# Performance work log

Measured on AMD Instinct MI355X. Metric: run time of the kernel, lower is better.

The kernel has to match this reference:

```python
import jax, jax.numpy as jnp
import numpy as np

N = 100000   # nodes
E = 1600000  # edges
D = 128      # input_dim == hidden_dim
L = 4        # n_layers
G = 128      # num graphs
NC = 10      # n_classes
EPS = 1e-5


def setup_inputs() -> dict:
    key = jax.random.key(0)
    ks = jax.random.split(key, 12)
    x = jax.random.normal(ks[0], (N, D), jnp.float32)
    edge_index = jax.random.randint(ks[1], (2, E), 0, N, dtype=jnp.int64)
    batch = jnp.sort(jax.random.randint(ks[2], (N,), 0, G, dtype=jnp.int64))
    s = 1.0 / np.sqrt(D)
    conv_w = jax.random.normal(ks[3], (L, D, D), jnp.float32) * s
    conv_b = jnp.zeros((L, D), jnp.float32)
    gn_weight = jnp.ones((L, D), jnp.float32)
    gn_bias = jnp.zeros((L, D), jnp.float32)
    gn_mean_scale = jnp.ones((L, D), jnp.float32)
    dense_w1 = jax.random.normal(ks[4], (D, D), jnp.float32) * s
    dense_b1 = jnp.zeros((D,), jnp.float32)
    bn_gamma = jnp.ones((D,), jnp.float32)
    bn_beta = jnp.zeros((D,), jnp.float32)
    bn_mean = jnp.zeros((D,), jnp.float32)   # running stats (eval mode)
    bn_var = jnp.ones((D,), jnp.float32)
    dense_w2 = jax.random.normal(ks[5], (D, NC), jnp.float32) * s
    dense_b2 = jnp.zeros((NC,), jnp.float32)
    return dict(x=x, edge_index=edge_index, batch=batch, conv_w=conv_w,
                conv_b=conv_b, gn_weight=gn_weight, gn_bias=gn_bias,
                gn_mean_scale=gn_mean_scale, dense_w1=dense_w1, dense_b1=dense_b1,
                bn_gamma=bn_gamma, bn_beta=bn_beta, bn_mean=bn_mean, bn_var=bn_var,
                dense_w2=dense_w2, dense_b2=dense_b2)


def _graph_norm(x, batch, counts, weight, bias, mean_scale):
    # PyG GraphNorm: (x - alpha*mean) / sqrt(var + eps) * weight + bias, per graph
    mean = jax.ops.segment_sum(x, batch, num_segments=G) / counts        # [G, D]
    sub = x - mean_scale * mean[batch]                                    # [N, D]
    var = jax.ops.segment_sum(sub * sub, batch, num_segments=G) / counts  # [G, D]
    return weight * sub * jax.lax.rsqrt(var + EPS)[batch] + bias


def reference(x, edge_index, batch, conv_w, conv_b, gn_weight, gn_bias,
              gn_mean_scale, dense_w1, dense_b1, bn_gamma, bn_beta,
              bn_mean, bn_var, dense_w2, dense_b2):
    # GCNConv normalization with self-loops (symmetric D^-1/2 (A+I) D^-1/2)
    loop = jnp.arange(N, dtype=edge_index.dtype)
    src = jnp.concatenate([edge_index[0], loop])
    dst = jnp.concatenate([edge_index[1], loop])
    deg = jax.ops.segment_sum(jnp.ones((E + N,), x.dtype), dst, num_segments=N)
    dis = jax.lax.rsqrt(deg)  # deg >= 1 due to self-loops
    nrm = (dis[src] * dis[dst])[:, None]                                  # [E+N, 1]
    counts = jax.ops.segment_sum(jnp.ones((N, 1), x.dtype), batch, num_segments=G)

    x_res = x  # input_dim == hidden_dim -> no input projection
    for i in range(L):
        h = x @ conv_w[i]                                # [N, D]
        h = jax.ops.segment_sum(h[src] * nrm, dst, num_segments=N) + conv_b[i]
        h = _graph_norm(h, batch, counts, gn_weight[i], gn_bias[i], gn_mean_scale[i])
        h = jax.nn.elu(h)
        # dropout: identity in eval mode
        x = h + x_res
        x_res = x

    pooled = jax.ops.segment_sum(x, batch, num_segments=G)  # global_add_pool [G, D]
    z = pooled @ dense_w1 + dense_b1
    z = bn_gamma * (z - bn_mean) * jax.lax.rsqrt(bn_var + EPS) + bn_beta
    z = jax.nn.relu(z)
    z = z @ dense_w2 + dense_b2
    return (x, z)
```

## Files before the change

kernel.cpp:

```cpp
#include <hip/hip_runtime.h>
#include <stdint.h>

#define N_NODES 100000
#define N_PAD   100032
#define N_EDGES 1600000
#define DIM 128
#define NLAYERS 4
#define NGRAPH 128
#define NCLS 10
#define EPSV 1e-5f
#define NSLOT 32

#define BIN_SHIFT 9
#define NBUCKET ((N_NODES + 511) >> 9)
#define P1_EPB 4096
#define P1_BLOCKS ((N_EDGES + P1_EPB - 1) / P1_EPB)

typedef __attribute__((ext_vector_type(8))) short short8_t;
typedef __attribute__((ext_vector_type(4))) float float4_t;


__device__ __forceinline__ float bf_lo(uint32_t u) { return __uint_as_float(u << 16); }
__device__ __forceinline__ float bf_hi(uint32_t u) { return __uint_as_float(u & 0xffff0000u); }
__device__ __forceinline__ uint32_t f2bf_rne(float f) {
    uint32_t x = __float_as_uint(f);
    return (x + 0x7fffu + ((x >> 16) & 1u)) >> 16;
}
__device__ __forceinline__ uint32_t pack_bf2(float a, float b) {
    return f2bf_rne(a) | (f2bf_rne(b) << 16);
}
__device__ __forceinline__ float4 unpack4(uint2 u) {
    return make_float4(bf_lo(u.x), bf_hi(u.x), bf_lo(u.y), bf_hi(u.y));
}
__device__ __forceinline__ float ub0(uint32_t u) { return (float)( u        & 0xffu); }
__device__ __forceinline__ float ub1(uint32_t u) { return (float)((u >>  8) & 0xffu); }
__device__ __forceinline__ float ub2(uint32_t u) { return (float)((u >> 16) & 0xffu); }
__device__ __forceinline__ float ub3(uint32_t u) { return (float)( u >> 24        ); }
__device__ __forceinline__ float elu_neg(float x) { return __expf(x) - 1.f; }


__global__ void k_node_meta(const int* __restrict__ batch, int* __restrict__ gstart,
                            int* __restrict__ bcnt) {
    int i = blockIdx.x * blockDim.x + threadIdx.x;
    if (i < NBUCKET) bcnt[i] = 0;
    if (i >= N_NODES) return;
    int b = batch[i];
    if (i == 0) {
        for (int g = 0; g <= b; g++) gstart[g] = 0;
    } else {
        int bp = batch[i - 1];
        for (int g = bp + 1; g <= b; g++) gstart[g] = i;
    }
    if (i == N_NODES - 1) {
        for (int g = b + 1; g <= NGRAPH; g++) gstart[g] = N_NODES;
    }
}

__global__ __launch_bounds__(256) void k_bhist(const int* __restrict__ ei, int* __restrict__ bcnt) {
    __shared__ int hist[NBUCKET];
    int t = threadIdx.x;
    for (int i = t; i < NBUCKET; i += 256) hist[i] = 0;
    __syncthreads();
    int e0 = blockIdx.x * P1_EPB;
    int e1 = e0 + P1_EPB; if (e1 > N_EDGES) e1 = N_EDGES;
    for (int e = e0 + t; e < e1; e += 256) atomicAdd(&hist[ei[N_EDGES + e] >> BIN_SHIFT], 1);
    __syncthreads();
    for (int i = t; i < NBUCKET; i += 256) if (hist[i]) atomicAdd(&bcnt[i], hist[i]);
}

__global__ __launch_bounds__(256) void k_bscan(const int* __restrict__ bcnt,
                                               int* __restrict__ bucket_off, int* __restrict__ bcur) {
    __shared__ int s[256];
    int t = threadIdx.x;
    int v = (t < NBUCKET) ? bcnt[t] : 0;
    s[t] = v; __syncthreads();
    for (int off = 1; off < 256; off <<= 1) {
        int a = (t >= off) ? s[t - off] : 0;
        __syncthreads();
        s[t] += a;
        __syncthreads();
    }
    if (t < NBUCKET) { bucket_off[t] = s[t] - v; bcur[t] = s[t] - v; }
    if (t == 0) bucket_off[NBUCKET] = s[255];
}

__global__ __launch_bounds__(256) void k_bin_edges(const int* __restrict__ ei,
                                                   int* __restrict__ bcur,
                                                   int2* __restrict__ binned) {
    __shared__ int hist[NBUCKET];
    __shared__ int base[NBUCKET];
    int t = threadIdx.x;
    int e0 = blockIdx.x * P1_EPB;
    int e1 = e0 + P1_EPB; if (e1 > N_EDGES) e1 = N_EDGES;
    for (int i = t; i < NBUCKET; i += 256) hist[i] = 0;
    __syncthreads();
    int myrank[P1_EPB / 256];
    int cnt = 0;
    for (int e = e0 + t; e < e1; e += 256) {
        int d = ei[N_EDGES + e];
        myrank[cnt++] = atomicAdd(&hist[d >> BIN_SHIFT], 1);
    }
    __syncthreads();
    for (int i = t; i < NBUCKET; i += 256) base[i] = atomicAdd(&bcur[i], hist[i]);
    __syncthreads();
    cnt = 0;
    for (int e = e0 + t; e < e1; e += 256) {
        int s = ei[e];
        int d = ei[N_EDGES + e];
        binned[base[d >> BIN_SHIFT] + myrank[cnt++]] = make_int2(s, d);
    }
}

__global__ __launch_bounds__(256) void k_bucket_build(const int2* __restrict__ binned,
                                                      const int* __restrict__ bucket_off,
                                                      int* __restrict__ rowoff,
                                                      float* __restrict__ dis,
                                                      int* __restrict__ psrc) {
    __shared__ int cnt[512];
    __shared__ int sa[512];
    __shared__ int sb[512];
    int b = blockIdx.x;
    int t = threadIdx.x;
    int n0 = b << BIN_SHIFT;
    int j0 = bucket_off[b], j1 = bucket_off[b + 1];
    cnt[t] = 0; cnt[t + 256] = 0;
    __syncthreads();
    for (int j = j0 + t; j < j1; j += 256) atomicAdd(&cnt[binned[j].y & 511], 1);
    __syncthreads();
    sa[t] = cnt[t]; sa[t + 256] = cnt[t + 256];
    __syncthreads();
    int* A = sa; int* B = sb;
    for (int off = 1; off < 512; off <<= 1) {
        int i0 = t, i1 = t + 256;
        B[i0] = A[i0] + ((i0 >= off) ? A[i0 - off] : 0);
        B[i1] = A[i1] + ((i1 >= off) ? A[i1 - off] : 0);
        __syncthreads();
        int* tmp = A; A = B; B = tmp;
    }
    for (int i = t; i < 512; i += 256) {
        int n = n0 + i;
        if (n < N_NODES) {
            rowoff[n] = j0 + A[i] - cnt[i];
            dis[n] = rsqrtf((float)(1 + cnt[i]));
        }
    }
    if (b == NBUCKET - 1 && t == 0) rowoff[N_NODES] = N_EDGES;
    for (int idx = t; idx < 512 * NSLOT; idx += 256) {
        int i = idx >> 5, k = idx & (NSLOT - 1);
        int n = n0 + i;
        if (n < N_NODES && k >= cnt[i]) psrc[(size_t)n * NSLOT + k] = N_NODES;
    }
}

__global__ __launch_bounds__(256) void k_scatter(const int2* __restrict__ binned,
                                                 const float* __restrict__ dis,
                                                 const int* __restrict__ rowoff,
                                                 const int* __restrict__ bucket_off,
                                                 int2* __restrict__ csc,
                                                 int* __restrict__ psrc) {
    __shared__ int lcur[512];
    int b = blockIdx.x;
    int t = threadIdx.x;
    lcur[t] = 0; lcur[t + 256] = 0;
    __syncthreads();
    int j0 = bucket_off[b], j1 = bucket_off[b + 1];
    for (int j = j0 + t; j < j1; j += 256) {
        int2 sd = binned[j];
        float w = dis[sd.x] * dis[sd.y];
        int rank = atomicAdd(&lcur[sd.y & 511], 1);
        csc[rowoff[sd.y] + rank] = make_int2(sd.x, __float_as_int(w));
        if (rank < NSLOT) psrc[(size_t)sd.y * NSLOT + rank] = sd.x;
    }
}

__global__ void k_cast_w(const float* __restrict__ W, uint32_t* __restrict__ Wt) {
    int i = blockIdx.x * blockDim.x + threadIdx.x;
    if (i >= NLAYERS * DIM * 64) return;
    int l = i / (DIM * 64);
    int n = (i / 64) % DIM;
    int ku = i % 64;
    const float* Wl = W + (size_t)l * DIM * DIM;
    float w0 = Wl[(2 * ku) * DIM + n];
    float w1 = Wl[(2 * ku + 1) * DIM + n];
    Wt[i] = pack_bf2(w0, w1);
}


__device__ __forceinline__ void gemm_phase(const uint32_t (*atile)[68], const uint32_t* __restrict__ Wt,
                                           uint8_t (*ctile8)[132], float* rmaxl,
                                           uint8_t* __restrict__ H8,
                                           float* __restrict__ hsd, const float* __restrict__ dis,
                                           int blk, int t) {
    int wid = t >> 6;
    int lane = t & 63;
    int quad = lane >> 4;
    int s15 = lane & 15;

    float4_t acc[8];
#pragma unroll
    for (int i = 0; i < 8; i++) acc[i] = (float4_t){0.f, 0.f, 0.f, 0.f};

#pragma unroll
    for (int kk = 0; kk < 4; kk++) {
        uint4 au = *(const uint4*)&atile[wid * 16 + s15][quad * 4 + kk * 16];
        short8_t a = __builtin_bit_cast(short8_t, au);
#pragma unroll
        for (int nt = 0; nt < 8; nt++) {
            uint4 bu = *(const uint4*)(Wt + (size_t)(nt * 16 + s15) * 64 + kk * 16 + quad * 4);
            short8_t b = __builtin_bit_cast(short8_t, bu);
            acc[nt] = __builtin_amdgcn_mfma_f32_16x16x32_bf16(a, b, acc[nt], 0, 0, 0);
        }
    }
    __syncthreads();

    float sinv[4];
#pragma unroll
    for (int r = 0; r < 4; r++) {
        float m = fabsf(acc[0][r]);
#pragma unroll
        for (int nt = 1; nt < 8; nt++) m = fmaxf(m, fabsf(acc[nt][r]));
        m = fmaxf(m, __shfl_xor(m, 1));
        m = fmaxf(m, __shfl_xor(m, 2));
        m = fmaxf(m, __shfl_xor(m, 4));
        m = fmaxf(m, __shfl_xor(m, 8));
        if (s15 == 0) rmaxl[wid * 16 + quad * 4 + r] = m;
        sinv[r] = (m > 0.f) ? 127.f / m : 0.f;
    }
#pragma unroll
    for (int nt = 0; nt < 8; nt++) {
#pragma unroll
        for (int r = 0; r < 4; r++) {
            int qv = (int)fmaf(acc[nt][r], sinv[r], 128.5f);
            ctile8[wid * 16 + quad * 4 + r][nt * 16 + s15] = (uint8_t)qv;
        }
    }
    __syncthreads();
    uint8_t* Hb = H8 + (size_t)blk * 64 * 128;
    float* Hsb = hsd + (size_t)blk * 64;
#pragma unroll
    for (int i = 0; i < 8; i++) {
        int idx = t + 256 * i;
        int row = idx >> 5, cu = idx & 31;
        uint32_t v = *(const uint32_t*)&ctile8[row][cu * 4];
        ((uint32_t*)Hb)[(size_t)row * 32 + cu] = v;
        if (cu == 0) {
            size_t gr = (size_t)blk * 64 + row;
            float dv = (gr < N_NODES) ? dis[gr] : 0.f;
            Hsb[row] = rmaxl[row] * (1.f / 127.f) * dv;
        }
    }
}

#define GEMM_SMEM \
    __shared__ __align__(16) char smem[64 * 68 * 4]; \
    uint32_t (*atile)[68] = (uint32_t(*)[68])smem; \
    uint8_t (*ctile8)[132] = (uint8_t(*)[132])smem; \
    float* rmaxl = (float*)(smem + 64 * 132);

__global__ __launch_bounds__(256) void k_gemm0(const float* __restrict__ X, const uint32_t* __restrict__ Wt,
                                               uint8_t* __restrict__ H8, float* __restrict__ hsd,
                                               const float* __restrict__ dis) {
    GEMM_SMEM
    int t = threadIdx.x;
    size_t row0 = (size_t)blockIdx.x * 64;
#pragma unroll
    for (int i = 0; i < 8; i++) {
        int idx = t + 256 * i;
        int row = idx >> 5, q = idx & 31;
        size_t gr = row0 + row;
        uint2 p = make_uint2(0u, 0u);
        if (gr < N_NODES) {
            float4 v = ((const float4*)(X + gr * DIM))[q];
            p.x = pack_bf2(v.x, v.y);
            p.y = pack_bf2(v.z, v.w);
        }
        *(uint2*)&atile[row][q * 2] = p;
    }
    __syncthreads();
    gemm_phase(atile, Wt, ctile8, rmaxl, H8, hsd, dis, blockIdx.x, t);
}

template <bool RBF>
__global__ __launch_bounds__(256) void k_norm_gemm(const uint32_t* __restrict__ A, const int* __restrict__ batch,
                                                   const float* __restrict__ amean, const float* __restrict__ rstd,
                                                   const float* __restrict__ gw, const float* __restrict__ gb,
                                                   const void* __restrict__ res, uint32_t* __restrict__ res_out,
                                                   const uint32_t* __restrict__ Wt,
                                                   uint8_t* __restrict__ H8, float* __restrict__ hsd,
                                                   const float* __restrict__ dis) {
    GEMM_SMEM
    int t = threadIdx.x;
    size_t row0 = (size_t)blockIdx.x * 64;
#pragma unroll
    for (int i = 0; i < 8; i++) {
        int idx = t + 256 * i;
        int row = idx >> 5, q = idx & 31;
        size_t gr = row0 + row;
        uint2 p = make_uint2(0u, 0u);
        if (gr < N_NODES) {
            int g = batch[gr];
            float4 v = unpack4(((const uint2*)(A + gr * 64))[q]);
            float4 am = ((const float4*)amean)[g * 32 + q];
            float4 rs = ((const float4*)rstd)[g * 32 + q];
            float4 w = ((const float4*)gw)[q];
            float4 b = ((const float4*)gb)[q];
            float4 r;
            if (RBF) r = unpack4(((const uint2*)((const uint32_t*)res + gr * 64))[q]);
            else     r = ((const float4*)res)[gr * 32 + q];
            float4 o;
            o.x = w.x * (v.x - am.x) * rs.x + b.x;
            o.y = w.y * (v.y - am.y) * rs.y + b.y;
            o.z = w.z * (v.z - am.z) * rs.z + b.z;
            o.w = w.w * (v.w - am.w) * rs.w + b.w;
            o.x = ((o.x > 0.f) ? o.x : elu_neg(o.x)) + r.x;
            o.y = ((o.y > 0.f) ? o.y : elu_neg(o.y)) + r.y;
            o.z = ((o.z > 0.f) ? o.z : elu_neg(o.z)) + r.z;
            o.w = ((o.w > 0.f) ? o.w : elu_neg(o.w)) + r.w;
            p.x = pack_bf2(o.x, o.y);
            p.y = pack_bf2(o.z, o.w);
            ((uint2*)(res_out + gr * 64))[q] = p;
        }
        *(uint2*)&atile[row][q * 2] = p;
    }
    __syncthreads();
    gemm_phase(atile, Wt, ctile8, rmaxl, H8, hsd, dis, blockIdx.x, t);
}


#define ACC8(WS, U) \
    acc[0] += WS * ub0(U.x); acc[1] += WS * ub1(U.x); \
    acc[2] += WS * ub2(U.x); acc[3] += WS * ub3(U.x); \
    acc[4] += WS * ub0(U.y); acc[5] += WS * ub1(U.y); \
    acc[6] += WS * ub2(U.y); acc[7] += WS * ub3(U.y);

__global__ __launch_bounds__(256, 4) void k_aggregate(const uint8_t* __restrict__ H8,
                                                      const float* __restrict__ hsd,
                                                      const int* __restrict__ psrc,
                                                      const int2* __restrict__ csc,
                                                      const int* __restrict__ rowoff,
                                                      const float* __restrict__ dis,
                                                      const float* __restrict__ bias,
                                                      uint32_t* __restrict__ Out) {
    int wid = threadIdx.x >> 6;
    int lane = threadIdx.x & 63;
    uint32_t q = (uint32_t)(lane >> 4);
    uint32_t s = (uint32_t)(lane & 15);
    uint32_t n = (uint32_t)blockIdx.x * 4u + (uint32_t)wid;
    uint32_t s8 = s << 3;

    float dd = dis[n];
    const int4* P = (const int4*)(psrc + ((size_t)n << 5) + (q << 3));
    int4 pa = P[0];
    int4 pb = P[1];
    float hn = hsd[n];
    uint2 us = *(const uint2*)(H8 + ((n << 7) | s8));
    int b0 = rowoff[n], b1 = rowoff[n + 1];

    float h0 = hsd[(uint32_t)pa.x];
    float h1 = hsd[(uint32_t)pa.y];
    float h2 = hsd[(uint32_t)pa.z];
    float h3 = hsd[(uint32_t)pa.w];
    float h4 = hsd[(uint32_t)pb.x];
    float h5 = hsd[(uint32_t)pb.y];
    float h6 = hsd[(uint32_t)pb.z];
    float h7 = hsd[(uint32_t)pb.w];
    uint2 u0 = *(const uint2*)(H8 + (((uint32_t)pa.x << 7) | s8));
    uint2 u1 = *(const uint2*)(H8 + (((uint32_t)pa.y << 7) | s8));
    uint2 u2 = *(const uint2*)(H8 + (((uint32_t)pa.z << 7) | s8));
    uint2 u3 = *(const uint2*)(H8 + (((uint32_t)pa.w << 7) | s8));
    uint2 u4 = *(const uint2*)(H8 + (((uint32_t)pb.x << 7) | s8));
    uint2 u5 = *(const uint2*)(H8 + (((uint32_t)pb.y << 7) | s8));
    uint2 u6 = *(const uint2*)(H8 + (((uint32_t)pb.z << 7) | s8));
    uint2 u7 = *(const uint2*)(H8 + (((uint32_t)pb.w << 7) | s8));

    float ws0 = dd * h0, ws1 = dd * h1, ws2 = dd * h2, ws3 = dd * h3;
    float ws4 = dd * h4, ws5 = dd * h5, ws6 = dd * h6, ws7 = dd * h7;

    float sw = (q == 0) ? dd * hn : 0.f;
    float acc[8];
    acc[0] = sw * ub0(us.x); acc[1] = sw * ub1(us.x);
    acc[2] = sw * ub2(us.x); acc[3] = sw * ub3(us.x);
    acc[4] = sw * ub0(us.y); acc[5] = sw * ub1(us.y);
    acc[6] = sw * ub2(us.y); acc[7] = sw * ub3(us.y);
    float offs = sw;

    ACC8(ws0, u0); ACC8(ws1, u1); ACC8(ws2, u2); ACC8(ws3, u3);
    ACC8(ws4, u4); ACC8(ws5, u5); ACC8(ws6, u6); ACC8(ws7, u7);
    offs += ws0 + ws1 + ws2 + ws3 + ws4 + ws5 + ws6 + ws7;

    if (b1 - b0 > NSLOT) {
        for (int j = b0 + NSLOT + (int)q; j < b1; j += 4) {
            uint32_t sx = (uint32_t)csc[j].x;
            float w = dd * hsd[sx];
            uint2 u = *(const uint2*)(H8 + ((sx << 7) | s8));
            ACC8(w, u);
            offs += w;
        }
    }

#pragma unroll
    for (int k = 0; k < 8; k++) {
        acc[k] += __shfl_xor(acc[k], 16);
        acc[k] += __shfl_xor(acc[k], 32);
    }
    offs += __shfl_xor(offs, 16);
    offs += __shfl_xor(offs, 32);
    float o0 = (q == 0) ? acc[0] : (q == 1) ? acc[2] : (q == 2) ? acc[4] : acc[6];
    float o1 = (q == 0) ? acc[1] : (q == 1) ? acc[3] : (q == 2) ? acc[5] : acc[7];
    float corr = -128.f * offs;
    float2 bb = ((const float2*)bias)[s * 4 + q];
    Out[(n << 6) | (s * 4 + q)] = pack_bf2(o0 + corr + bb.x, o1 + corr + bb.y);
}

__global__ __launch_bounds__(512) void k_stats(const uint32_t* __restrict__ A, const int* __restrict__ gstart,
                                               const float* __restrict__ mscale,
                                               float* __restrict__ amean, float* __restrict__ rstd) {
    __shared__ float L1[8][DIM];
    __shared__ float L2[8][DIM];
    int g = blockIdx.x;
    int t = threadIdx.x;
    int f2 = t & 63;
    int p = t >> 6;
    int s0 = gstart[g], s1 = gstart[g + 1];
    float sa = 0.f, sb = 0.f, qa = 0.f, qb = 0.f;
    for (int n = s0 + p; n < s1; n += 8) {
        uint32_t u = A[(size_t)n * 64 + f2];
        float a = bf_lo(u), b = bf_hi(u);
        sa += a; qa += a * a;
        sb += b; qb += b * b;
    }
    L1[p][2 * f2] = sa; L1[p][2 * f2 + 1] = sb;
    L2[p][2 * f2] = qa; L2[p][2 * f2 + 1] = qb;
    __syncthreads();
    if (t < DIM) {
        float s = 0.f, s2 = 0.f;
#pragma unroll
        for (int i = 0; i < 8; i++) { s += L1[i][t]; s2 += L2[i][t]; }
        int cnt = s1 - s0;
        float inv = (cnt > 0) ? 1.0f / (float)cnt : 0.f;
        float m = s * inv;
        float a = mscale[t];
        float var = s2 * inv - (2.f * a - a * a) * m * m;
        amean[g * DIM + t] = a * m;
        rstd[g * DIM + t] = rsqrtf(var + EPSV);
    }
}

__global__ __launch_bounds__(512) void k_pool_head(const uint32_t* __restrict__ A,
                                                   const uint32_t* __restrict__ resb,
                                                   const int* __restrict__ gstart,
                                                   const float* __restrict__ amean, const float* __restrict__ rstd,
                                                   const float* __restrict__ gw, const float* __restrict__ gb,
                                                   const float* __restrict__ w1, const float* __restrict__ b1,
                                                   const float* __restrict__ gamma, const float* __restrict__ beta,
                                                   const float* __restrict__ rmean, const float* __restrict__ rvar,
                                                   const float* __restrict__ w2, const float* __restrict__ b2,
                                                   float* __restrict__ outx, float* __restrict__ zout) {
    __shared__ float L[8][DIM];
    __shared__ float sp[DIM];
    __shared__ float sz[DIM];
    int g = blockIdx.x, t = threadIdx.x;
    int f2 = t & 63;
    int p = t >> 6;
    int s0 = gstart[g], s1 = gstart[g + 1];
    float am0 = amean[g * DIM + 2 * f2], am1 = amean[g * DIM + 2 * f2 + 1];
    float rs0 = rstd[g * DIM + 2 * f2],  rs1 = rstd[g * DIM + 2 * f2 + 1];
    float w0_ = gw[2 * f2], w1_ = gw[2 * f2 + 1];
    float b0_ = gb[2 * f2], b1_ = gb[2 * f2 + 1];
    float p0 = 0.f, p1 = 0.f;
    for (int n = s0 + p; n < s1; n += 8) {
        uint32_t u = A[(size_t)n * 64 + f2];
        uint32_t ur = resb[(size_t)n * 64 + f2];
        float a = bf_lo(u), b = bf_hi(u);
        float r0 = bf_lo(ur), r1 = bf_hi(ur);
        float o0 = w0_ * (a - am0) * rs0 + b0_;
        float o1 = w1_ * (b - am1) * rs1 + b1_;
        o0 = ((o0 > 0.f) ? o0 : elu_neg(o0)) + r0;
        o1 = ((o1 > 0.f) ? o1 : elu_neg(o1)) + r1;
        ((float2*)(outx + (size_t)n * DIM))[f2] = make_float2(o0, o1);
        p0 += o0; p1 += o1;
    }
    L[p][2 * f2] = p0; L[p][2 * f2 + 1] = p1;
    __syncthreads();
    if (t < DIM) {
        float s = 0.f;
#pragma unroll
        for (int i = 0; i < 8; i++) s += L[i][t];
        sp[t] = s;
    }
    __syncthreads();
    if (t < DIM) {
        float acc = b1[t];
#pragma unroll 8
        for (int k = 0; k < DIM; k++) acc += sp[k] * w1[k * DIM + t];
        acc = gamma[t] * (acc - rmean[t]) * rsqrtf(rvar[t] + EPSV) + beta[t];
        sz[t] = fmaxf(acc, 0.f);
    }
    __syncthreads();
    if (t < NCLS) {
        float a2 = b2[t];
#pragma unroll 8
        for (int k = 0; k < DIM; k++) a2 += sz[k] * w2[k * NCLS + t];
        zout[g * NCLS + t] = a2;
    }
}


extern "C" void kernel_launch(void* const* d_in, const int* in_sizes, int n_in,
                              void* d_out, int out_size, void* d_ws, size_t ws_size,
                              hipStream_t stream) {
    const float* x_in   = (const float*)d_in[0];
    const int*   ei     = (const int*)d_in[1];
    const int*   batch  = (const int*)d_in[2];
    const float* conv_w = (const float*)d_in[3];
    const float* conv_b = (const float*)d_in[4];
    const float* gn_w   = (const float*)d_in[5];
    const float* gn_b   = (const float*)d_in[6];
    const float* gn_ms  = (const float*)d_in[7];
    const float* w1     = (const float*)d_in[8];
    const float* b1     = (const float*)d_in[9];
    const float* bng    = (const float*)d_in[10];
    const float* bnb    = (const float*)d_in[11];
    const float* bnm    = (const float*)d_in[12];
    const float* bnv    = (const float*)d_in[13];
    const float* w2     = (const float*)d_in[14];
    const float* b2     = (const float*)d_in[15];

    float* out_x = (float*)d_out;
    float* out_z = out_x + (size_t)N_NODES * DIM;

    char* ws = (char*)d_ws;
    size_t off = 0;
    auto alloc = [&](size_t bytes) -> void* {
        void* p = ws + off;
        off += (bytes + 255) / 256 * 256;
        return p;
    };
    uint8_t* h8      = (uint8_t*)alloc(sizeof(uint8_t) * (size_t)N_PAD * 128);
    float*   hsd     = (float*)alloc(sizeof(float) * (size_t)N_PAD);
    uint32_t* agg    = (uint32_t*)alloc(sizeof(uint32_t) * (size_t)N_NODES * 64);
    uint32_t* resb   = (uint32_t*)alloc(sizeof(uint32_t) * (size_t)N_NODES * 64);
    int2*  csc       = (int2*)alloc(sizeof(int2) * (size_t)N_EDGES);
    int2*  binned    = (int2*)alloc(sizeof(int2) * (size_t)N_EDGES);
    int*   psrc      = (int*)alloc(sizeof(int) * (size_t)N_NODES * NSLOT);
    uint32_t* wt     = (uint32_t*)alloc(sizeof(uint32_t) * NLAYERS * DIM * 64);
    float* dis       = (float*)alloc(sizeof(float) * N_NODES);
    int*   rowoff    = (int*)alloc(sizeof(int) * (N_NODES + 1));
    int*   bcnt      = (int*)alloc(sizeof(int) * NBUCKET);
    int*   boffb     = (int*)alloc(sizeof(int) * (NBUCKET + 1));
    int*   bcur      = (int*)alloc(sizeof(int) * NBUCKET);
    int*   gstart    = (int*)alloc(sizeof(int) * (NGRAPH + 1));
    float* amean     = (float*)alloc(sizeof(float) * NGRAPH * DIM);
    float* rstd      = (float*)alloc(sizeof(float) * NGRAPH * DIM);

    k_node_meta<<<(N_NODES + 255) / 256, 256, 0, stream>>>(batch, gstart, bcnt);
    k_bhist<<<P1_BLOCKS, 256, 0, stream>>>(ei, bcnt);
    k_bscan<<<1, 256, 0, stream>>>(bcnt, boffb, bcur);
    k_bin_edges<<<P1_BLOCKS, 256, 0, stream>>>(ei, bcur, binned);
    k_bucket_build<<<NBUCKET, 256, 0, stream>>>(binned, boffb, rowoff, dis, psrc);
    k_scatter<<<NBUCKET, 256, 0, stream>>>(binned, dis, rowoff, boffb, csc, psrc);
    k_cast_w<<<(NLAYERS * DIM * 64 + 255) / 256, 256, 0, stream>>>(conv_w, wt);

    k_gemm0<<<N_PAD / 64, 256, 0, stream>>>(x_in, wt, h8, hsd, dis);
    for (int l = 0; l < NLAYERS; l++) {
        k_aggregate<<<N_NODES / 4, 256, 0, stream>>>(h8, hsd, psrc, csc, rowoff, dis,
                                                     conv_b + (size_t)l * DIM, agg);
        k_stats<<<NGRAPH, 512, 0, stream>>>(agg, gstart, gn_ms + (size_t)l * DIM, amean, rstd);
        if (l == 0) {
            k_norm_gemm<false><<<N_PAD / 64, 256, 0, stream>>>(agg, batch, amean, rstd, gn_w, gn_b,
                                                               (const void*)x_in, resb,
                                                               wt + (size_t)1 * DIM * 64, h8, hsd, dis);
        } else if (l < NLAYERS - 1) {
            k_norm_gemm<true><<<N_PAD / 64, 256, 0, stream>>>(agg, batch, amean, rstd,
                                                              gn_w + (size_t)l * DIM, gn_b + (size_t)l * DIM,
                                                              (const void*)resb, resb,
                                                              wt + (size_t)(l + 1) * DIM * 64, h8, hsd, dis);
        } else {
            k_pool_head<<<NGRAPH, 512, 0, stream>>>(agg, resb, gstart, amean, rstd,
                                                    gn_w + (size_t)l * DIM, gn_b + (size_t)l * DIM,
                                                    w1, b1, bng, bnb, bnm, bnv, w2, b2, out_x, out_z);
        }
    }
}
```

Baseline: 771.9 us.

## Process two nodes per wavefront in aggregation and fold self-loop into padded slots

```diff
diff --git a/kernel.cpp b/kernel.cpp
--- a/kernel.cpp
+++ b/kernel.cpp
@@ -148,7 +148,7 @@
     for (int idx = t; idx < 512 * NSLOT; idx += 256) {
         int i = idx >> 5, k = idx & (NSLOT - 1);
         int n = n0 + i;
-        if (n < N_NODES && k >= cnt[i]) psrc[(size_t)n * NSLOT + k] = N_NODES;
+        if (n < N_NODES && k >= cnt[i]) psrc[(size_t)n * NSLOT + k] = (k == cnt[i]) ? n : N_NODES;
     }
 }
 
@@ -343,27 +343,20 @@
                                                       uint32_t* __restrict__ Out) {
     int wid = threadIdx.x >> 6;
     int lane = threadIdx.x & 63;
-    uint32_t q = (uint32_t)(lane >> 4);
-    uint32_t s = (uint32_t)(lane & 15);
-    uint32_t n = (uint32_t)blockIdx.x * 4u + (uint32_t)wid;
+    uint32_t hq = (uint32_t)((lane >> 4) & 1);
+    uint32_t s  = (uint32_t)(lane & 15);
+    uint32_t n  = (uint32_t)blockIdx.x * 8u + ((uint32_t)wid << 1) + (uint32_t)(lane >> 5);
     uint32_t s8 = s << 3;
 
     float dd = dis[n];
-    const int4* P = (const int4*)(psrc + ((size_t)n << 5) + (q << 3));
-    int4 pa = P[0];
-    int4 pb = P[1];
-    float hn = hsd[n];
-    uint2 us = *(const uint2*)(H8 + ((n << 7) | s8));
     int b0 = rowoff[n], b1 = rowoff[n + 1];
-
-    float h0 = hsd[(uint32_t)pa.x];
-    float h1 = hsd[(uint32_t)pa.y];
-    float h2 = hsd[(uint32_t)pa.z];
-    float h3 = hsd[(uint32_t)pa.w];
-    float h4 = hsd[(uint32_t)pb.x];
-    float h5 = hsd[(uint32_t)pb.y];
-    float h6 = hsd[(uint32_t)pb.z];
-    float h7 = hsd[(uint32_t)pb.w];
+    const int4* P = (const int4*)(psrc + ((size_t)n << 5) + (hq << 4));
+    int4 pa = P[0], pb = P[1], pc = P[2], pd = P[3];
+
+    float h0 = hsd[(uint32_t)pa.x], h1 = hsd[(uint32_t)pa.y];
+    float h2 = hsd[(uint32_t)pa.z], h3 = hsd[(uint32_t)pa.w];
+    float h4 = hsd[(uint32_t)pb.x], h5 = hsd[(uint32_t)pb.y];
+    float h6 = hsd[(uint32_t)pb.z], h7 = hsd[(uint32_t)pb.w];
     uint2 u0 = *(const uint2*)(H8 + (((uint32_t)pa.x << 7) | s8));
     uint2 u1 = *(const uint2*)(H8 + (((uint32_t)pa.y << 7) | s8));
     uint2 u2 = *(const uint2*)(H8 + (((uint32_t)pa.z << 7) | s8));
@@ -373,25 +366,40 @@
     uint2 u6 = *(const uint2*)(H8 + (((uint32_t)pb.z << 7) | s8));
     uint2 u7 = *(const uint2*)(H8 + (((uint32_t)pb.w << 7) | s8));
 
-    float ws0 = dd * h0, ws1 = dd * h1, ws2 = dd * h2, ws3 = dd * h3;
-    float ws4 = dd * h4, ws5 = dd * h5, ws6 = dd * h6, ws7 = dd * h7;
-
-    float sw = (q == 0) ? dd * hn : 0.f;
     float acc[8];
-    acc[0] = sw * ub0(us.x); acc[1] = sw * ub1(us.x);
-    acc[2] = sw * ub2(us.x); acc[3] = sw * ub3(us.x);
-    acc[4] = sw * ub0(us.y); acc[5] = sw * ub1(us.y);
-    acc[6] = sw * ub2(us.y); acc[7] = sw * ub3(us.y);
-    float offs = sw;
-
-    ACC8(ws0, u0); ACC8(ws1, u1); ACC8(ws2, u2); ACC8(ws3, u3);
-    ACC8(ws4, u4); ACC8(ws5, u5); ACC8(ws6, u6); ACC8(ws7, u7);
-    offs += ws0 + ws1 + ws2 + ws3 + ws4 + ws5 + ws6 + ws7;
-
-    if (b1 - b0 > NSLOT) {
-        for (int j = b0 + NSLOT + (int)q; j < b1; j += 4) {
+#pragma unroll
+    for (int k = 0; k < 8; k++) acc[k] = 0.f;
+
+    ACC8(h0, u0); ACC8(h1, u1); ACC8(h2, u2); ACC8(h3, u3);
+    ACC8(h4, u4); ACC8(h5, u5); ACC8(h6, u6); ACC8(h7, u7);
+
+    float h8  = hsd[(uint32_t)pc.x], h9  = hsd[(uint32_t)pc.y];
+    float h10 = hsd[(uint32_t)pc.z], h11 = hsd[(uint32_t)pc.w];
+    float h12 = hsd[(uint32_t)pd.x], h13 = hsd[(uint32_t)pd.y];
+    float h14 = hsd[(uint32_t)pd.z], h15 = hsd[(uint32_t)pd.w];
+    uint2 u8  = *(const uint2*)(H8 + (((uint32_t)pc.x << 7) | s8));
+    uint2 u9  = *(const uint2*)(H8 + (((uint32_t)pc.y << 7) | s8));
+    uint2 u10 = *(const uint2*)(H8 + (((uint32_t)pc.z << 7) | s8));
+    uint2 u11 = *(const uint2*)(H8 + (((uint32_t)pc.w << 7) | s8));
+    uint2 u12 = *(const uint2*)(H8 + (((uint32_t)pd.x << 7) | s8));
+    uint2 u13 = *(const uint2*)(H8 + (((uint32_t)pd.y << 7) | s8));
+    uint2 u14 = *(const uint2*)(H8 + (((uint32_t)pd.z << 7) | s8));
+    uint2 u15 = *(const uint2*)(H8 + (((uint32_t)pd.w << 7) | s8));
+
+    ACC8(h8, u8);  ACC8(h9, u9);  ACC8(h10, u10); ACC8(h11, u11);
+    ACC8(h12, u12); ACC8(h13, u13); ACC8(h14, u14); ACC8(h15, u15);
+
+    float offs = ((h0 + h1) + (h2 + h3)) + ((h4 + h5) + (h6 + h7))
+               + ((h8 + h9) + (h10 + h11)) + ((h12 + h13) + (h14 + h15));
+
+    if (b1 - b0 >= NSLOT) {
+        float wsf = (hq == 0) ? hsd[n] : 0.f;
+        uint2 uu = *(const uint2*)(H8 + ((n << 7) | s8));
+        ACC8(wsf, uu);
+        offs += wsf;
+        for (int j = b0 + NSLOT + (int)hq; j < b1; j += 2) {
             uint32_t sx = (uint32_t)csc[j].x;
-            float w = dd * hsd[sx];
+            float w = hsd[sx];
             uint2 u = *(const uint2*)(H8 + ((sx << 7) | s8));
             ACC8(w, u);
             offs += w;
@@ -399,17 +407,19 @@
     }
 
 #pragma unroll
-    for (int k = 0; k < 8; k++) {
-        acc[k] += __shfl_xor(acc[k], 16);
-        acc[k] += __shfl_xor(acc[k], 32);
-    }
+    for (int k = 0; k < 8; k++) acc[k] += __shfl_xor(acc[k], 16);
     offs += __shfl_xor(offs, 16);
-    offs += __shfl_xor(offs, 32);
-    float o0 = (q == 0) ? acc[0] : (q == 1) ? acc[2] : (q == 2) ? acc[4] : acc[6];
-    float o1 = (q == 0) ? acc[1] : (q == 1) ? acc[3] : (q == 2) ? acc[5] : acc[7];
+
     float corr = -128.f * offs;
-    float2 bb = ((const float2*)bias)[s * 4 + q];
-    Out[(n << 6) | (s * 4 + q)] = pack_bf2(o0 + corr + bb.x, o1 + corr + bb.y);
+    float a0 = hq ? acc[4] : acc[0];
+    float a1 = hq ? acc[5] : acc[1];
+    float a2 = hq ? acc[6] : acc[2];
+    float a3 = hq ? acc[7] : acc[3];
+    float4 bb = ((const float4*)bias)[(s << 1) | hq];
+    uint2 ov;
+    ov.x = pack_bf2(fmaf(dd, a0 + corr, bb.x), fmaf(dd, a1 + corr, bb.y));
+    ov.y = pack_bf2(fmaf(dd, a2 + corr, bb.z), fmaf(dd, a3 + corr, bb.w));
+    *(uint2*)(Out + ((n << 6) | (s << 2) | (hq << 1))) = ov;
 }
 
 __global__ __launch_bounds__(512) void k_stats(const uint32_t* __restrict__ A, const int* __restrict__ gstart,
@@ -563,7 +573,7 @@
 
     k_gemm0<<<N_PAD / 64, 256, 0, stream>>>(x_in, wt, h8, hsd, dis);
     for (int l = 0; l < NLAYERS; l++) {
-        k_aggregate<<<N_NODES / 4, 256, 0, stream>>>(h8, hsd, psrc, csc, rowoff, dis,
+        k_aggregate<<<N_NODES / 8, 256, 0, stream>>>(h8, hsd, psrc, csc, rowoff, dis,
                                                      conv_b + (size_t)l * DIM, agg);
         k_stats<<<NGRAPH, 512, 0, stream>>>(agg, gstart, gn_ms + (size_t)l * DIM, amean, rstd);
         if (l == 0) {
```

New measurement: 737.8 us. 4.4% less time.
